# Performance work log

Hardware: AMD Instinct MI355X
Metric: run time of the kernel (lower is better)

The kernel has to match this reference:

```python
import jax, jax.numpy as jnp
import numpy as np

DINO_SHIFT = 0.7
COEF = 1.0
EPS = 1e-12


def setup_inputs() -> dict:
    key = jax.random.key(0)
    k1, k2 = jax.random.split(key)
    N, H, W, C, K = 2, 48, 48, 384, 16
    dino_feature_map = jax.random.normal(k1, (N, H, W, C), dtype=jnp.float32)
    # relevance map in log space (log-probabilities over classes)
    log_p_class = jax.nn.log_softmax(jax.random.normal(k2, (N, H, W, K), dtype=jnp.float32), axis=-1)
    dino_pos_weight = jnp.ones((1,), dtype=jnp.float32)
    dino_neg_weight = jnp.ones((1,), dtype=jnp.float32)
    return {
        "dino_feature_map": dino_feature_map,
        "log_p_class": log_p_class,
        "dino_pos_weight": dino_pos_weight,
        "dino_neg_weight": dino_neg_weight,
    }


def _normalize(x):
    # F.normalize(x, dim=-1): x / max(||x||, eps)
    n = jnp.sqrt(jnp.sum(x * x, axis=-1, keepdims=True))
    return x / jnp.maximum(n, EPS)


def _js_correlation(a, b):
    # a, b: [N, L, C] log-probs. Pairwise JS divergence matrix [N, L, L].
    # Same math as the torch broadcast version, but the sum over C is
    # factored into einsums so the [N,L,L,C] tensor is never materialized:
    #   kl_am[s,l] = sum_c e^{a[s,c]} a[s,c] - sum_c e^{a[s,c]} m[l,c]
    m = jnp.logaddexp(a, b) - jnp.log(2.0)           # [N, L, C]
    ea = jnp.exp(a)
    kl_am = jnp.sum(ea * a, axis=-1)[:, :, None] - jnp.einsum('nsc,nlc->nsl', ea, m)
    eb = jnp.exp(b)
    kl_bm = jnp.sum(eb * b, axis=-1)[:, :, None] - jnp.einsum('nsc,nlc->nsl', eb, m)
    return (kl_am + kl_bm) / 2.0


def _fda_loss(feats, log_p, pw, nw):
    N = feats.shape[0]
    f = feats.reshape(N, -1, feats.shape[-1])          # [N, HW, C]
    p = log_p.reshape(N, -1, log_p.shape[-1])          # [N, HW, K]
    fn = _normalize(f)
    f_corr = jnp.einsum('nsc,nlc->nsl', fn, fn) - DINO_SHIFT
    f_corr = jax.lax.stop_gradient(f_corr)             # torch.no_grad block
    f_pos = jnp.maximum(f_corr, 0.0)
    f_neg = jnp.minimum(f_corr, 0.0)
    p_corr = _js_correlation(p, p)                     # [N, HW, HW]
    n_pos = jnp.count_nonzero(f_pos).astype(f_pos.dtype)
    n_neg = jnp.count_nonzero(f_neg).astype(f_neg.dtype)
    pos_loss = jnp.sum(f_pos * p_corr) / n_pos
    neg_loss = jnp.sum(f_neg * p_corr) / n_neg
    loss = pos_loss * pw[0] + neg_loss * nw[0]
    return loss * COEF                                 # reduction='none' on a scalar


def reference(dino_feature_map, log_p_class, dino_pos_weight, dino_neg_weight):
    return _fda_loss(dino_feature_map, log_p_class, dino_pos_weight, dino_neg_weight)
```

## Files before the change

kernel.cpp:

```cpp
#include <hip/hip_runtime.h>
#include <math.h>
#include <stdint.h>

#define NN 2
#define LL 2304
#define CC 384
#define KK 16
#define DINO_SHIFT 0.7f

#define NT 24
#define TB 96
#define TT ((NT * (NT + 1)) / 2)
#define NBLK2 (NN * TT)

typedef __attribute__((ext_vector_type(8))) short short8;
typedef __attribute__((ext_vector_type(4))) float f32x4;
typedef __attribute__((ext_vector_type(2))) float f32x2;

#define AS_G __attribute__((address_space(1)))
#define AS_L __attribute__((address_space(3)))

__device__ __forceinline__ unsigned short f2bf(float x) {
    union { float f; uint32_t u; } v; v.f = x;
    uint32_t r = v.u + 0x7fffu + ((v.u >> 16) & 1u);
    return (unsigned short)(r >> 16);
}

__device__ __forceinline__ unsigned int f2e4m3(float x) {
    unsigned int u = __float_as_uint(x);
    unsigned int s = (u >> 24) & 0x80u;
    unsigned int au = u & 0x7fffffffu;
    unsigned int code;
    if (au < 0x3C800000u) {
        code = (unsigned int)__builtin_rintf(__uint_as_float(au) * 512.0f);
    } else {
        unsigned int lsb = (au >> 20) & 1u;
        au += 0x7FFFFu + lsb;
        code = (au >> 20) - (120u << 3);
    }
    return s | code;
}
__device__ __forceinline__ unsigned short fp8pair(float a, float b) {
#if __has_builtin(__builtin_amdgcn_cvt_pk_fp8_f32)
    return (unsigned short)(__builtin_amdgcn_cvt_pk_fp8_f32(a, b, 0, false) & 0xffff);
#else
    return (unsigned short)(f2e4m3(a) | (f2e4m3(b) << 8));
#endif
}

__device__ __forceinline__ void gll16(const void* g, void* l) {
    __builtin_amdgcn_global_load_lds((const AS_G unsigned int*)g,
                                     (AS_L unsigned int*)l, 16, 0, 0);
}

__global__ void prep_kernel(const float* __restrict__ f, const float* __restrict__ p,
                            unsigned char* __restrict__ fnorm8,
                            unsigned short* __restrict__ Ppad,
                            unsigned short* __restrict__ ppad,
                            float* __restrict__ selfdot) {
    const int r = blockIdx.x * 4 + (threadIdx.x >> 6);
    const int lane = threadIdx.x & 63;
    const f32x2* frow2 = (const f32x2*)(f + (size_t)r * CC);
    f32x2 v[3];
    float ss = 0.f;
#pragma unroll
    for (int k = 0; k < 3; ++k) {
        v[k] = frow2[lane + 64 * k];
        ss = fmaf(v[k][0], v[k][0], fmaf(v[k][1], v[k][1], ss));
    }
#pragma unroll
    for (int off = 32; off; off >>= 1) ss += __shfl_xor(ss, off);
    const float rn = 1.0f / fmaxf(sqrtf(ss), 1e-12f);
    unsigned short* fr = (unsigned short*)(fnorm8 + (size_t)r * CC);
#pragma unroll
    for (int k = 0; k < 3; ++k)
        fr[lane + 64 * k] = fp8pair(v[k][0] * rn, v[k][1] * rn);

    if (lane < 32) {
        float pv = 0.f, e = 0.f;
        if (lane < KK) { pv = p[(size_t)r * KK + lane]; e = expf(pv); }
        Ppad[(size_t)r * 32 + lane] = (lane < KK) ? f2bf(e)  : (unsigned short)0;
        ppad[(size_t)r * 32 + lane] = (lane < KK) ? f2bf(pv) : (unsigned short)0;
        float sd = e * pv;
#pragma unroll
        for (int off = 8; off; off >>= 1) sd += __shfl_xor(sd, off, 16);
        if (lane == 0) selfdot[r] = sd;
    }
}

__global__ __launch_bounds__(256, 2) void pair_kernel(
    const unsigned char* __restrict__ fnorm8,
    const unsigned short* __restrict__ Ppad, const unsigned short* __restrict__ ppad,
    const float* __restrict__ selfdot, float* __restrict__ partials)
{
    __shared__ char lds[73728] __attribute__((aligned(16)));
    __shared__ float red[4][4];

    const int b = blockIdx.x;
    const int n = b / TT;
    int t = b % TT;
    int i = 0;
    while (t >= NT - i) { t -= NT - i; ++i; }
    const int j = i + t;
    const int s0 = i * TB, l0 = j * TB;
    const bool diag = (i == j);
    const float wgt = diag ? 1.f : 2.f;

    const int tid = threadIdx.x, lane = tid & 63, w = tid >> 6;
    const int wrow = w >> 1, wcol = w & 1;

    const unsigned char* fn = fnorm8 + (size_t)n * LL * CC;

#pragma unroll
    for (int q = 0; q < 9; ++q) {
        const int slot = tid + 256 * q;
        const int row = slot / 24;
        const int jj = slot % 24;
        const int g = jj >> 3, c = jj & 7;
        gll16(fn + (size_t)(s0 + row) * CC + g * 128 + ((c ^ (row & 7)) << 4),
              lds + slot * 16);
    }
    if (!diag) {
#pragma unroll
        for (int q = 0; q < 9; ++q) {
            const int slot = tid + 256 * q;
            const int row = slot / 24;
            const int jj = slot % 24;
            const int g = jj >> 3, c = jj & 7;
            gll16(fn + (size_t)(l0 + row) * CC + g * 128 + ((c ^ (row & 7)) << 4),
                  lds + 36864 + slot * 16);
        }
    }

    short8 a2[3], b2[3];
    f32x4 sd4[3];
#pragma unroll
    for (int im = 0; im < 3; ++im) {
        const int row = wrow * 48 + im * 16 + (lane & 15);
        a2[im] = *(const short8*)((const char*)Ppad
                  + (size_t)(n * LL + s0 + row) * 64 + ((lane >> 4) << 4));
        sd4[im] = *(const f32x4*)(selfdot + (size_t)n * LL + s0
                  + wrow * 48 + im * 16 + ((lane >> 4) << 2));
    }
#pragma unroll
    for (int jn = 0; jn < 3; ++jn) {
        const int row = wcol * 48 + jn * 16 + (lane & 15);
        b2[jn] = *(const short8*)((const char*)ppad
                  + (size_t)(n * LL + l0 + row) * 64 + ((lane >> 4) << 4));
    }

    __syncthreads();

    const char* abase = lds;
    const char* bbase = diag ? lds : lds + 36864;
    f32x4 acc[3][3] = {};
#pragma unroll
    for (int kt = 0; kt < 3; ++kt) {
#pragma unroll
        for (int ks = 0; ks < 4; ++ks) {
            const int unit = ks * 2 + ((lane >> 5) & 1);
            const int w8 = ((lane >> 4) & 1) * 8;
            long a[3], bb[3];
#pragma unroll
            for (int im = 0; im < 3; ++im) {
                const int row = wrow * 48 + im * 16 + (lane & 15);
                a[im] = *(const long*)(abase + row * 384 + kt * 128
                         + ((unit ^ (row & 7)) << 4) + w8);
            }
#pragma unroll
            for (int jn = 0; jn < 3; ++jn) {
                const int row = wcol * 48 + jn * 16 + (lane & 15);
                bb[jn] = *(const long*)(bbase + row * 384 + kt * 128
                         + ((unit ^ (row & 7)) << 4) + w8);
            }
#pragma unroll
            for (int im = 0; im < 3; ++im)
#pragma unroll
                for (int jn = 0; jn < 3; ++jn)
                    acc[im][jn] = __builtin_amdgcn_mfma_f32_16x16x32_fp8_fp8(
                        a[im], bb[jn], acc[im][jn], 0, 0, 0);
        }
    }

    float pos = 0.f, neg = 0.f, npc = 0.f, nnc = 0.f;
#pragma unroll
    for (int im = 0; im < 3; ++im) {
#pragma unroll
        for (int jn = 0; jn < 3; ++jn) {
            f32x4 z = {0.f, 0.f, 0.f, 0.f};
            f32x4 pdv = __builtin_amdgcn_mfma_f32_16x16x32_bf16(a2[im], b2[jn], z, 0, 0, 0);
#pragma unroll
            for (int r = 0; r < 4; ++r) {
                const float fc = acc[im][jn][r] - DINO_SHIFT;
                const float pc = sd4[im][r] - pdv[r];
                const float v = fc * pc;
                if (fc > 0.f)      { pos += v; npc += 1.f; }
                else if (fc < 0.f) { neg += v; nnc += 1.f; }
            }
        }
    }
    pos *= wgt; neg *= wgt; npc *= wgt; nnc *= wgt;

#pragma unroll
    for (int off = 32; off; off >>= 1) {
        pos += __shfl_xor(pos, off); neg += __shfl_xor(neg, off);
        npc += __shfl_xor(npc, off); nnc += __shfl_xor(nnc, off);
    }
    if (lane == 0) { red[w][0] = pos; red[w][1] = neg; red[w][2] = npc; red[w][3] = nnc; }
    __syncthreads();
    if (tid == 0) {
        partials[b * 4 + 0] = red[0][0] + red[1][0] + red[2][0] + red[3][0];
        partials[b * 4 + 1] = red[0][1] + red[1][1] + red[2][1] + red[3][1];
        partials[b * 4 + 2] = red[0][2] + red[1][2] + red[2][2] + red[3][2];
        partials[b * 4 + 3] = red[0][3] + red[1][3] + red[2][3] + red[3][3];
    }
}

__global__ void final_kernel(const float* __restrict__ partials,
                             const float* __restrict__ pw,
                             const float* __restrict__ nw,
                             float* __restrict__ out) {
    __shared__ float red[4][4];
    const int tid = threadIdx.x;
    float pos = 0.f, neg = 0.f, np = 0.f, nn = 0.f;
    for (int i = tid; i < NBLK2; i += 256) {
        const f32x4 v = *(const f32x4*)(partials + i * 4);
        pos += v[0]; neg += v[1]; np += v[2]; nn += v[3];
    }
#pragma unroll
    for (int off = 32; off; off >>= 1) {
        pos += __shfl_xor(pos, off); neg += __shfl_xor(neg, off);
        np  += __shfl_xor(np, off);  nn  += __shfl_xor(nn, off);
    }
    const int w = tid >> 6, lane = tid & 63;
    if (lane == 0) { red[w][0] = pos; red[w][1] = neg; red[w][2] = np; red[w][3] = nn; }
    __syncthreads();
    if (tid == 0) {
        pos = red[0][0] + red[1][0] + red[2][0] + red[3][0];
        neg = red[0][1] + red[1][1] + red[2][1] + red[3][1];
        np  = red[0][2] + red[1][2] + red[2][2] + red[3][2];
        nn  = red[0][3] + red[1][3] + red[2][3] + red[3][3];
        out[0] = (pos / np) * pw[0] + (neg / nn) * nw[0];
    }
}

extern "C" void kernel_launch(void* const* d_in, const int* in_sizes, int n_in,
                              void* d_out, int out_size, void* d_ws, size_t ws_size,
                              hipStream_t stream) {
    const float* f  = (const float*)d_in[0];
    const float* p  = (const float*)d_in[1];
    const float* pw = (const float*)d_in[2];
    const float* nw = (const float*)d_in[3];
    float* out = (float*)d_out;

    unsigned char* fnorm8 = (unsigned char*)d_ws;
    unsigned short* Ppad  = (unsigned short*)(fnorm8 + (size_t)NN * LL * CC);
    unsigned short* ppad  = Ppad + (size_t)NN * LL * 32;
    float* selfdot  = (float*)(ppad + (size_t)NN * LL * 32);
    float* partials = selfdot + (size_t)NN * LL;

    prep_kernel<<<(NN * LL) / 4, 256, 0, stream>>>(f, p, fnorm8, Ppad, ppad, selfdot);
    pair_kernel<<<NBLK2, 256, 0, stream>>>(fnorm8, Ppad, ppad, selfdot, partials);
    final_kernel<<<1, 256, 0, stream>>>(partials, pw, nw, out);
}
```

Baseline: 25.33 us.

## Assign one 48x48 triangular tile per wave, loading fp8 operands directly from global

Drops the 96x96 block tiles staged in LDS via global_load_lds. Each wavefront now owns one 48x48 upper-triangular tile and reads fp8 MFMA operands straight from global memory into registers, with no LDS and no block barriers. Partials are written per wave, and the final kernel reduces over four times as many entries. This removes the LDS staging, the sync and the occupancy limit, but adds redundant global/L2 traffic because operand rows are no longer shared across waves, and reads use strided uncoalesced 8-byte loads.

```diff
diff --git a/kernel.cpp b/kernel.cpp
--- a/kernel.cpp
+++ b/kernel.cpp
@@ -8,17 +8,15 @@
 #define KK 16
 #define DINO_SHIFT 0.7f
 
-#define NT 24
-#define TB 96
-#define TT ((NT * (NT + 1)) / 2)
-#define NBLK2 (NN * TT)
+#define NTW 48
+#define TB 48
+#define TTW ((NTW * (NTW + 1)) / 2)
+#define NWAVE (NN * TTW)
+#define NBLK2 (NWAVE / 4)
 
 typedef __attribute__((ext_vector_type(8))) short short8;
 typedef __attribute__((ext_vector_type(4))) float f32x4;
 typedef __attribute__((ext_vector_type(2))) float f32x2;
-
-#define AS_G __attribute__((address_space(1)))
-#define AS_L __attribute__((address_space(3)))
 
 __device__ __forceinline__ unsigned short f2bf(float x) {
     union { float f; uint32_t u; } v; v.f = x;
@@ -48,11 +46,6 @@
 #endif
 }
 
-__device__ __forceinline__ void gll16(const void* g, void* l) {
-    __builtin_amdgcn_global_load_lds((const AS_G unsigned int*)g,
-                                     (AS_L unsigned int*)l, 16, 0, 0);
-}
-
 __global__ void prep_kernel(const float* __restrict__ f, const float* __restrict__ p,
                             unsigned char* __restrict__ fnorm8,
                             unsigned short* __restrict__ Ppad,
@@ -88,91 +81,45 @@
     }
 }
 
-__global__ __launch_bounds__(256, 2) void pair_kernel(
+__global__ __launch_bounds__(256) void pair_kernel(
     const unsigned char* __restrict__ fnorm8,
     const unsigned short* __restrict__ Ppad, const unsigned short* __restrict__ ppad,
     const float* __restrict__ selfdot, float* __restrict__ partials)
 {
-    __shared__ char lds[73728] __attribute__((aligned(16)));
-    __shared__ float red[4][4];
-
-    const int b = blockIdx.x;
-    const int n = b / TT;
-    int t = b % TT;
+    const int gid = blockIdx.x * 4 + (threadIdx.x >> 6);
+    const int lane = threadIdx.x & 63;
+    const int n = gid / TTW;
+    int t = gid % TTW;
     int i = 0;
-    while (t >= NT - i) { t -= NT - i; ++i; }
+    while (t >= NTW - i) { t -= NTW - i; ++i; }
     const int j = i + t;
     const int s0 = i * TB, l0 = j * TB;
-    const bool diag = (i == j);
-    const float wgt = diag ? 1.f : 2.f;
-
-    const int tid = threadIdx.x, lane = tid & 63, w = tid >> 6;
-    const int wrow = w >> 1, wcol = w & 1;
+    const float wgt = (i == j) ? 1.f : 2.f;
 
     const unsigned char* fn = fnorm8 + (size_t)n * LL * CC;
-
-#pragma unroll
-    for (int q = 0; q < 9; ++q) {
-        const int slot = tid + 256 * q;
-        const int row = slot / 24;
-        const int jj = slot % 24;
-        const int g = jj >> 3, c = jj & 7;
-        gll16(fn + (size_t)(s0 + row) * CC + g * 128 + ((c ^ (row & 7)) << 4),
-              lds + slot * 16);
-    }
-    if (!diag) {
-#pragma unroll
-        for (int q = 0; q < 9; ++q) {
-            const int slot = tid + 256 * q;
-            const int row = slot / 24;
-            const int jj = slot % 24;
-            const int g = jj >> 3, c = jj & 7;
-            gll16(fn + (size_t)(l0 + row) * CC + g * 128 + ((c ^ (row & 7)) << 4),
-                  lds + 36864 + slot * 16);
-        }
-    }
-
-    short8 a2[3], b2[3];
-    f32x4 sd4[3];
-#pragma unroll
-    for (int im = 0; im < 3; ++im) {
-        const int row = wrow * 48 + im * 16 + (lane & 15);
-        a2[im] = *(const short8*)((const char*)Ppad
-                  + (size_t)(n * LL + s0 + row) * 64 + ((lane >> 4) << 4));
-        sd4[im] = *(const f32x4*)(selfdot + (size_t)n * LL + s0
-                  + wrow * 48 + im * 16 + ((lane >> 4) << 2));
-    }
-#pragma unroll
-    for (int jn = 0; jn < 3; ++jn) {
-        const int row = wcol * 48 + jn * 16 + (lane & 15);
-        b2[jn] = *(const short8*)((const char*)ppad
-                  + (size_t)(n * LL + l0 + row) * 64 + ((lane >> 4) << 4));
-    }
-
-    __syncthreads();
-
-    const char* abase = lds;
-    const char* bbase = diag ? lds : lds + 36864;
+    const int r15 = lane & 15;
+    const int koff = (lane >> 4) * 8;
+
+    const unsigned char* ab[3];
+    const unsigned char* bbp[3];
+#pragma unroll
+    for (int im = 0; im < 3; ++im)
+        ab[im] = fn + (size_t)(s0 + im * 16 + r15) * CC + koff;
+#pragma unroll
+    for (int jn = 0; jn < 3; ++jn)
+        bbp[jn] = fn + (size_t)(l0 + jn * 16 + r15) * CC + koff;
+
     f32x4 acc[3][3] = {};
 #pragma unroll
     for (int kt = 0; kt < 3; ++kt) {
 #pragma unroll
         for (int ks = 0; ks < 4; ++ks) {
-            const int unit = ks * 2 + ((lane >> 5) & 1);
-            const int w8 = ((lane >> 4) & 1) * 8;
+            const int off = kt * 128 + ks * 32;
             long a[3], bb[3];
 #pragma unroll
-            for (int im = 0; im < 3; ++im) {
-                const int row = wrow * 48 + im * 16 + (lane & 15);
-                a[im] = *(const long*)(abase + row * 384 + kt * 128
-                         + ((unit ^ (row & 7)) << 4) + w8);
-            }
-#pragma unroll
-            for (int jn = 0; jn < 3; ++jn) {
-                const int row = wcol * 48 + jn * 16 + (lane & 15);
-                bb[jn] = *(const long*)(bbase + row * 384 + kt * 128
-                         + ((unit ^ (row & 7)) << 4) + w8);
-            }
+            for (int im = 0; im < 3; ++im) a[im] = *(const long*)(ab[im] + off);
+#pragma unroll
+            for (int jn = 0; jn < 3; ++jn) bb[jn] = *(const long*)(bbp[jn] + off);
 #pragma unroll
             for (int im = 0; im < 3; ++im)
 #pragma unroll
@@ -180,6 +127,21 @@
                     acc[im][jn] = __builtin_amdgcn_mfma_f32_16x16x32_fp8_fp8(
                         a[im], bb[jn], acc[im][jn], 0, 0, 0);
         }
+    }
+
+    short8 a2[3], b2[3];
+    f32x4 sd4[3];
+#pragma unroll
+    for (int im = 0; im < 3; ++im) {
+        a2[im] = *(const short8*)((const char*)Ppad
+                  + (size_t)(n * LL + s0 + im * 16 + r15) * 64 + ((lane >> 4) << 4));
+        sd4[im] = *(const f32x4*)(selfdot + (size_t)n * LL + s0
+                  + im * 16 + ((lane >> 4) << 2));
+    }
+#pragma unroll
+    for (int jn = 0; jn < 3; ++jn) {
+        b2[jn] = *(const short8*)((const char*)ppad
+                  + (size_t)(n * LL + l0 + jn * 16 + r15) * 64 + ((lane >> 4) << 4));
     }
 
     float pos = 0.f, neg = 0.f, npc = 0.f, nnc = 0.f;
@@ -199,20 +161,15 @@
             }
         }
     }
-    pos *= wgt; neg *= wgt; npc *= wgt; nnc *= wgt;
 
 #pragma unroll
     for (int off = 32; off; off >>= 1) {
         pos += __shfl_xor(pos, off); neg += __shfl_xor(neg, off);
         npc += __shfl_xor(npc, off); nnc += __shfl_xor(nnc, off);
     }
-    if (lane == 0) { red[w][0] = pos; red[w][1] = neg; red[w][2] = npc; red[w][3] = nnc; }
-    __syncthreads();
-    if (tid == 0) {
-        partials[b * 4 + 0] = red[0][0] + red[1][0] + red[2][0] + red[3][0];
-        partials[b * 4 + 1] = red[0][1] + red[1][1] + red[2][1] + red[3][1];
-        partials[b * 4 + 2] = red[0][2] + red[1][2] + red[2][2] + red[3][2];
-        partials[b * 4 + 3] = red[0][3] + red[1][3] + red[2][3] + red[3][3];
+    if (lane == 0) {
+        f32x4 o = {pos * wgt, neg * wgt, npc * wgt, nnc * wgt};
+        *(f32x4*)(partials + (size_t)gid * 4) = o;
     }
 }
 
@@ -223,8 +180,8 @@
     __shared__ float red[4][4];
     const int tid = threadIdx.x;
     float pos = 0.f, neg = 0.f, np = 0.f, nn = 0.f;
-    for (int i = tid; i < NBLK2; i += 256) {
-        const f32x4 v = *(const f32x4*)(partials + i * 4);
+    for (int i = tid; i < NWAVE; i += 256) {
+        const f32x4 v = *(const f32x4*)(partials + (size_t)i * 4);
         pos += v[0]; neg += v[1]; np += v[2]; nn += v[3];
     }
 #pragma unroll
```

Result: slower. 42.16 us (+66.5%).
